# Kernel tuning notes

Measured on AMD Instinct MI355X. Metric: run time of the kernel, lower is better.

Reference implementation:

```python
import jax, jax.numpy as jnp
import numpy as np

SEQ_LEN = 8192
D_K = 128
NEG_BIG = 1000000000.0


def setup_inputs() -> dict:
    key = jax.random.key(0)
    kq, kk, kv = jax.random.split(key, 3)
    q = jax.random.normal(kq, (SEQ_LEN, D_K), dtype=jnp.float32)
    k = jax.random.normal(kk, (SEQ_LEN, D_K), dtype=jnp.float32)
    v = jax.random.normal(kv, (SEQ_LEN, D_K), dtype=jnp.float32)
    return {"q": q, "k": k, "v": v}


def reference(q, k, v):
    # q,k,v: (S, d). Naive attention with causal (look-ahead) mask, masked=True.
    d_k = q.shape[-1]
    scaled_logits = jnp.matmul(q, k.T) / jnp.sqrt(jnp.asarray(d_k, q.dtype))  # (S, S)
    look_ahead_mask = jnp.triu(jnp.ones((SEQ_LEN, SEQ_LEN), dtype=q.dtype), k=1)
    scaled_logits = scaled_logits - look_ahead_mask * NEG_BIG
    attn = jnp.matmul(jax.nn.softmax(scaled_logits, axis=-1), v)  # (S, d)
    return attn
```

## Files before the change

kernel.cpp:

```cpp
#include <hip/hip_runtime.h>
#include <hip/hip_bf16.h>
#include <math.h>

#define S_LEN 8192
#define DK    128
#define BM    64
#define BN    64
#define NQT   (S_LEN / BM)
#define SCALE 0.08838834764831845f

typedef __bf16 bf16x8_t __attribute__((ext_vector_type(8)));
typedef __bf16 bf16x4_t __attribute__((ext_vector_type(4)));
typedef float  floatx4  __attribute__((ext_vector_type(4)));

#define GLD16(g, l) __builtin_amdgcn_global_load_lds(                      \
    (const __attribute__((address_space(1))) void*)(g),                    \
    (__attribute__((address_space(3))) void*)(l), 16, 0, 0)

__global__ __launch_bounds__(256) void prep_k(const float* __restrict__ K,
                                              __bf16* __restrict__ Kb) {
  const int i = (blockIdx.x * 256 + threadIdx.x) * 4;
  float4 v = *(const float4*)&K[i];
  bf16x4_t b;
  b[0] = (__bf16)v.x; b[1] = (__bf16)v.y; b[2] = (__bf16)v.z; b[3] = (__bf16)v.w;
  *(bf16x4_t*)&Kb[i] = b;
}

__global__ __launch_bounds__(256) void prep_vt(const float* __restrict__ V,
                                               __bf16* __restrict__ Vt) {
  __shared__ __bf16 t[64][DK + 8];
  const int tid  = threadIdx.x;
  const int key0 = blockIdx.x * 64;
  {
    const int r = tid >> 2, cg = (tid & 3) * 32;
    const float* vp = V + (size_t)(key0 + r) * DK + cg;
    #pragma unroll
    for (int i = 0; i < 8; ++i) {
      float4 v = ((const float4*)vp)[i];
      bf16x4_t b;
      b[0] = (__bf16)v.x; b[1] = (__bf16)v.y; b[2] = (__bf16)v.z; b[3] = (__bf16)v.w;
      *(bf16x4_t*)&t[r][cg + i * 4] = b;
    }
  }
  __syncthreads();
  const int d = tid >> 1, h = (tid & 1) * 32;
  __bf16* op = Vt + (size_t)d * S_LEN + key0 + h;
  #pragma unroll
  for (int jb = 0; jb < 4; ++jb) {
    bf16x8_t b;
    #pragma unroll
    for (int j = 0; j < 8; ++j) b[j] = t[h + jb * 8 + j][d];
    *(bf16x8_t*)&op[jb * 8] = b;
  }
}

__global__ __launch_bounds__(256, 3)
void fa_part(const float* __restrict__ Q, const __bf16* __restrict__ Kb,
             const __bf16* __restrict__ Vtg, float* __restrict__ Opart,
             float* __restrict__ stats, int G, int direct) {
  __shared__ __align__(16) __bf16 Ks[BN * DK];
  __shared__ __align__(16) __bf16 Vts[DK * BN];
  __shared__ __align__(16) __bf16 Pl[4][16][BN + 8];

  const int tid  = threadIdx.x;
  const int wave = tid >> 6;
  const int lane = tid & 63;
  const int l15  = lane & 15;
  const int quad = lane >> 4;

  const int qtile = blockIdx.x;
  const int g     = blockIdx.y;
  const int nt    = qtile + 1;
  const int Ci    = (nt + G - 1) / G;
  const int jb0   = g * Ci;
  const int jb1   = (jb0 + Ci < nt) ? (jb0 + Ci) : nt;
  const int chunk = qtile * G + g;

  if (jb0 >= jb1) {
    if (tid < BM) {
      stats[((size_t)chunk * BM + tid) * 2 + 0] = -INFINITY;
      stats[((size_t)chunk * BM + tid) * 2 + 1] = 0.f;
    }
    return;
  }

  const int q0w = qtile * BM + wave * 16;

  bf16x8_t qf[4];
  {
    const float* qrow = Q + (size_t)(q0w + l15) * DK + quad * 8;
    #pragma unroll
    for (int kb = 0; kb < 4; ++kb) {
      const float4* p = (const float4*)(qrow + kb * 32);
      float4 a = p[0], b = p[1];
      bf16x8_t f;
      f[0]=(__bf16)a.x; f[1]=(__bf16)a.y; f[2]=(__bf16)a.z; f[3]=(__bf16)a.w;
      f[4]=(__bf16)b.x; f[5]=(__bf16)b.y; f[6]=(__bf16)b.z; f[7]=(__bf16)b.w;
      qf[kb] = f;
    }
  }

  const __bf16* kp[4]; const __bf16* vp[4];
  __bf16* kl[4]; __bf16* vl[4];
  {
    const int ck = l15 ^ ((wave * 4 + (lane >> 4)) & 15);
    const int cv = (lane & 7) ^ ((lane >> 3) & 7);
    #pragma unroll
    for (int t = 0; t < 4; ++t) {
      const int rk = t * 16 + wave * 4 + (lane >> 4);
      kp[t] = Kb + ((size_t)(jb0 * BN + rk)) * DK + ck * 8;
      kl[t] = &Ks[t * 2048 + wave * 512];
      const int rv = t * 32 + wave * 8 + (lane >> 3);
      vp[t] = Vtg + (size_t)rv * S_LEN + jb0 * BN + cv * 8;
      vl[t] = &Vts[t * 2048 + wave * 512];
    }
  }

  floatx4 o_acc[8];
  #pragma unroll
  for (int dt = 0; dt < 8; ++dt) o_acc[dt] = (floatx4){0.f, 0.f, 0.f, 0.f};
  float m_r[4], l_r[4];
  #pragma unroll
  for (int r = 0; r < 4; ++r) { m_r[r] = -INFINITY; l_r[r] = 0.f; }

  for (int jb = jb0; jb < jb1; ++jb) {
    const int key0 = jb * BN;

    #pragma unroll
    for (int t = 0; t < 4; ++t) {
      GLD16(kp[t], kl[t]);
      GLD16(vp[t], vl[t]);
      kp[t] += BN * DK;
      vp[t] += BN;
    }
    __syncthreads();

    floatx4 sv[4];
    #pragma unroll
    for (int n = 0; n < 4; ++n) {
      floatx4 acc = (floatx4){0.f, 0.f, 0.f, 0.f};
      #pragma unroll
      for (int kb = 0; kb < 4; ++kb) {
        bf16x8_t bfr = *(const bf16x8_t*)
            &Ks[(n * 16 + l15) * DK + (((kb * 4 + quad) ^ l15) * 8)];
        acc = __builtin_amdgcn_mfma_f32_16x16x32_bf16(qf[kb], bfr, acc, 0, 0, 0);
      }
      sv[n] = acc;
    }

    if (jb == qtile) {
      #pragma unroll
      for (int n = 0; n < 4; ++n) {
        const int key = key0 + n * 16 + l15;
        #pragma unroll
        for (int r = 0; r < 4; ++r) {
          const int qi = q0w + quad * 4 + r;
          float v = sv[n][r] * SCALE;
          sv[n][r] = (key > qi) ? -1e30f : v;
        }
      }
    } else {
      #pragma unroll
      for (int n = 0; n < 4; ++n)
        #pragma unroll
        for (int r = 0; r < 4; ++r) sv[n][r] *= SCALE;
    }

    float rm[4];
    #pragma unroll
    for (int r = 0; r < 4; ++r)
      rm[r] = fmaxf(fmaxf(sv[0][r], sv[1][r]), fmaxf(sv[2][r], sv[3][r]));
    #pragma unroll
    for (int off = 8; off >= 1; off >>= 1) {
      #pragma unroll
      for (int r = 0; r < 4; ++r) rm[r] = fmaxf(rm[r], __shfl_xor(rm[r], off));
    }
    float alpha[4];
    #pragma unroll
    for (int r = 0; r < 4; ++r) {
      const float mn = fmaxf(m_r[r], rm[r]);
      alpha[r] = __expf(m_r[r] - mn);
      m_r[r] = mn;
    }
    float rs[4] = {0.f, 0.f, 0.f, 0.f};
    #pragma unroll
    for (int n = 0; n < 4; ++n) {
      #pragma unroll
      for (int r = 0; r < 4; ++r) {
        const float p = __expf(sv[n][r] - m_r[r]);
        sv[n][r] = p;
        rs[r] += p;
      }
    }
    #pragma unroll
    for (int off = 8; off >= 1; off >>= 1) {
      #pragma unroll
      for (int r = 0; r < 4; ++r) rs[r] += __shfl_xor(rs[r], off);
    }
    #pragma unroll
    for (int r = 0; r < 4; ++r) l_r[r] = l_r[r] * alpha[r] + rs[r];
    #pragma unroll
    for (int dt = 0; dt < 8; ++dt)
      #pragma unroll
      for (int r = 0; r < 4; ++r) o_acc[dt][r] *= alpha[r];

    #pragma unroll
    for (int n = 0; n < 4; ++n)
      #pragma unroll
      for (int r = 0; r < 4; ++r)
        Pl[wave][quad * 4 + r][n * 16 + l15] = (__bf16)sv[n][r];
    __syncthreads();

    #pragma unroll
    for (int kc = 0; kc < 2; ++kc) {
      bf16x8_t af = *(const bf16x8_t*)&Pl[wave][l15][kc * 32 + quad * 8];
      #pragma unroll
      for (int dt = 0; dt < 8; ++dt) {
        bf16x8_t vf = *(const bf16x8_t*)
            &Vts[(dt * 16 + l15) * BN + (((kc * 4 + quad) ^ (l15 & 7)) * 8)];
        o_acc[dt] = __builtin_amdgcn_mfma_f32_16x16x32_bf16(af, vf, o_acc[dt], 0, 0, 0);
      }
    }
    __syncthreads();
  }

  if (direct) {
    #pragma unroll
    for (int r = 0; r < 4; ++r) {
      const float inv = 1.0f / l_r[r];
      float* orow = Opart + (size_t)(q0w + quad * 4 + r) * DK + l15;
      #pragma unroll
      for (int dt = 0; dt < 8; ++dt) orow[dt * 16] = o_acc[dt][r] * inv;
    }
  } else {
    #pragma unroll
    for (int r = 0; r < 4; ++r) {
      const int row = wave * 16 + quad * 4 + r;
      float* orow = Opart + ((size_t)chunk * BM + row) * DK + l15;
      #pragma unroll
      for (int dt = 0; dt < 8; ++dt) orow[dt * 16] = o_acc[dt][r];
    }
    if (l15 == 0) {
      #pragma unroll
      for (int r = 0; r < 4; ++r) {
        const int row = wave * 16 + quad * 4 + r;
        stats[((size_t)chunk * BM + row) * 2 + 0] = m_r[r];
        stats[((size_t)chunk * BM + row) * 2 + 1] = l_r[r];
      }
    }
  }
}

__global__ __launch_bounds__(256)
void fa_reduce(const float* __restrict__ Opart, const float* __restrict__ stats,
               float* __restrict__ O, int G) {
  const int wave = threadIdx.x >> 6, lane = threadIdx.x & 63;
  const int row = blockIdx.x * 4 + wave;
  const int qt = row >> 6, r = row & 63;

  float M = -INFINITY;
  for (int g = 0; g < G; ++g)
    M = fmaxf(M, stats[((size_t)(qt * G + g) * BM + r) * 2]);

  float L = 0.f;
  float ax = 0.f, ay = 0.f;
  for (int g = 0; g < G; ++g) {
    const size_t sidx = (size_t)(qt * G + g) * BM + r;
    const float m = stats[sidx * 2];
    if (m == -INFINITY) continue;
    const float w = __expf(m - M);
    L += stats[sidx * 2 + 1] * w;
    float2 o = *(const float2*)&Opart[sidx * DK + lane * 2];
    ax += w * o.x; ay += w * o.y;
  }
  const float inv = 1.f / L;
  float2 res; res.x = ax * inv; res.y = ay * inv;
  *(float2*)&O[(size_t)row * DK + lane * 2] = res;
}

extern "C" void kernel_launch(void* const* d_in, const int* in_sizes, int n_in,
                              void* d_out, int out_size, void* d_ws, size_t ws_size,
                              hipStream_t stream) {
  (void)in_sizes; (void)n_in; (void)out_size;
  const float* q = (const float*)d_in[0];
  const float* k = (const float*)d_in[1];
  const float* v = (const float*)d_in[2];
  float* out = (float*)d_out;

  const size_t conv_bytes = (size_t)S_LEN * DK * 2 * 2;
  const size_t per_g = (size_t)NQT * (BM * DK + 2 * BM) * 4;
  int G = 1;
  if (ws_size > conv_bytes + per_g) {
    G = (int)((ws_size - conv_bytes) / per_g);
    if (G > 8) G = 8;
  }

  __bf16* Kb = (__bf16*)d_ws;
  __bf16* Vt = Kb + (size_t)S_LEN * DK;
  float* Opart = (float*)(Vt + (size_t)S_LEN * DK);
  float* stats = Opart + (size_t)NQT * G * BM * DK;

  prep_k<<<(S_LEN * DK) / (256 * 4), 256, 0, stream>>>(k, Kb);
  prep_vt<<<S_LEN / 64, 256, 0, stream>>>(v, Vt);

  if (G >= 2) {
    fa_part<<<dim3(NQT, G), 256, 0, stream>>>(q, Kb, Vt, Opart, stats, G, 0);
    fa_reduce<<<S_LEN / 4, 256, 0, stream>>>(Opart, stats, out, G);
  } else {
    fa_part<<<dim3(NQT, 1), 256, 0, stream>>>(q, Kb, Vt, out, out, 1, 1);
  }
}
```

Before: 137.0 us.

## Fixed-size key chunks, K double-buffering, exp2 softmax, lazy rescale, fused prep

Splits each query tile's key range into fixed-size chunks of C tiles rather than G equal splits, launching heaviest tiles first. K is double-buffered in LDS so the next tile's load overlaps compute. Softmax switches to exp2 with the log2e factor folded into the scale, rescales only when some row max grows, and computes row sums via an MFMA against a ones vector. It also fuses the K and V prep kernels, adds s_setprio around MFMA blocks, and drops occupancy hint to 2, trading extra LDS for overlap.

```diff
diff --git a/kernel.cpp b/kernel.cpp
--- a/kernel.cpp
+++ b/kernel.cpp
@@ -7,7 +7,7 @@
 #define BM    64
 #define BN    64
 #define NQT   (S_LEN / BM)
-#define SCALE 0.08838834764831845f
+#define SCALE2 (0.08838834764831845f * 1.4426950408889634f)
 
 typedef __bf16 bf16x8_t __attribute__((ext_vector_type(8)));
 typedef __bf16 bf16x4_t __attribute__((ext_vector_type(4)));
@@ -17,20 +17,30 @@
     (const __attribute__((address_space(1))) void*)(g),                    \
     (__attribute__((address_space(3))) void*)(l), 16, 0, 0)
 
-__global__ __launch_bounds__(256) void prep_k(const float* __restrict__ K,
-                                              __bf16* __restrict__ Kb) {
-  const int i = (blockIdx.x * 256 + threadIdx.x) * 4;
-  float4 v = *(const float4*)&K[i];
-  bf16x4_t b;
-  b[0] = (__bf16)v.x; b[1] = (__bf16)v.y; b[2] = (__bf16)v.z; b[3] = (__bf16)v.w;
-  *(bf16x4_t*)&Kb[i] = b;
-}
-
-__global__ __launch_bounds__(256) void prep_vt(const float* __restrict__ V,
+__device__ __forceinline__ float fexp2(float x) {
+#if __has_builtin(__builtin_amdgcn_exp2f)
+  return __builtin_amdgcn_exp2f(x);
+#else
+  return exp2f(x);
+#endif
+}
+
+__global__ __launch_bounds__(256) void prep_kv(const float* __restrict__ K,
+                                               const float* __restrict__ V,
+                                               __bf16* __restrict__ Kb,
                                                __bf16* __restrict__ Vt) {
   __shared__ __bf16 t[64][DK + 8];
-  const int tid  = threadIdx.x;
-  const int key0 = blockIdx.x * 64;
+  const int bx  = blockIdx.x;
+  const int tid = threadIdx.x;
+  if (bx < (S_LEN * DK) / (256 * 4)) {
+    const int i = (bx * 256 + tid) * 4;
+    float4 v = *(const float4*)&K[i];
+    bf16x4_t b;
+    b[0] = (__bf16)v.x; b[1] = (__bf16)v.y; b[2] = (__bf16)v.z; b[3] = (__bf16)v.w;
+    *(bf16x4_t*)&Kb[i] = b;
+    return;
+  }
+  const int key0 = (bx - (S_LEN * DK) / (256 * 4)) * 64;
   {
     const int r = tid >> 2, cg = (tid & 3) * 32;
     const float* vp = V + (size_t)(key0 + r) * DK + cg;
@@ -54,12 +64,12 @@
   }
 }
 
-__global__ __launch_bounds__(256, 3)
+__global__ __launch_bounds__(256, 2)
 void fa_part(const float* __restrict__ Q, const __bf16* __restrict__ Kb,
              const __bf16* __restrict__ Vtg, float* __restrict__ Opart,
-             float* __restrict__ stats, int G, int direct) {
-  __shared__ __align__(16) __bf16 Ks[BN * DK];
-  __shared__ __align__(16) __bf16 Vts[DK * BN];
+             float* __restrict__ stats, int C, int direct) {
+  __shared__ __align__(16) __bf16 Ks[2][BN * DK];
+  __shared__ __align__(16) __bf16 Vts[BN * DK];
   __shared__ __align__(16) __bf16 Pl[4][16][BN + 8];
 
   const int tid  = threadIdx.x;
@@ -68,21 +78,15 @@
   const int l15  = lane & 15;
   const int quad = lane >> 4;
 
-  const int qtile = blockIdx.x;
+  const int qtile = (NQT - 1) - blockIdx.x;
   const int g     = blockIdx.y;
   const int nt    = qtile + 1;
-  const int Ci    = (nt + G - 1) / G;
-  const int jb0   = g * Ci;
-  const int jb1   = (jb0 + Ci < nt) ? (jb0 + Ci) : nt;
-  const int chunk = qtile * G + g;
-
-  if (jb0 >= jb1) {
-    if (tid < BM) {
-      stats[((size_t)chunk * BM + tid) * 2 + 0] = -INFINITY;
-      stats[((size_t)chunk * BM + tid) * 2 + 1] = 0.f;
-    }
-    return;
-  }
+  const int ca    = qtile / C;
+  if (g > ca) return;
+  const int cr  = qtile - ca * C;
+  const int jb0 = g * C;
+  const int jb1 = (jb0 + C < nt) ? (jb0 + C) : nt;
+  const int chunk = qtile + C * (ca * (ca - 1) / 2) + cr * ca + g;
 
   const int q0w = qtile * BM + wave * 16;
 
@@ -100,19 +104,17 @@
     }
   }
 
-  const __bf16* kp[4]; const __bf16* vp[4];
-  __bf16* kl[4]; __bf16* vl[4];
+  const __bf16* kp[4]; const __bf16* vp[4]; int loff[4];
   {
-    const int ck = l15 ^ ((wave * 4 + (lane >> 4)) & 15);
+    const int ck = l15 ^ ((wave * 4 + quad) & 15);
     const int cv = (lane & 7) ^ ((lane >> 3) & 7);
     #pragma unroll
     for (int t = 0; t < 4; ++t) {
-      const int rk = t * 16 + wave * 4 + (lane >> 4);
+      const int rk = t * 16 + wave * 4 + quad;
       kp[t] = Kb + ((size_t)(jb0 * BN + rk)) * DK + ck * 8;
-      kl[t] = &Ks[t * 2048 + wave * 512];
       const int rv = t * 32 + wave * 8 + (lane >> 3);
       vp[t] = Vtg + (size_t)rv * S_LEN + jb0 * BN + cv * 8;
-      vl[t] = &Vts[t * 2048 + wave * 512];
+      loff[t] = t * 2048 + wave * 512;
     }
   }
 
@@ -123,47 +125,56 @@
   #pragma unroll
   for (int r = 0; r < 4; ++r) { m_r[r] = -INFINITY; l_r[r] = 0.f; }
 
+  bf16x8_t onesf;
+  #pragma unroll
+  for (int j = 0; j < 8; ++j) onesf[j] = (__bf16)1.0f;
+
+  #pragma unroll
+  for (int t = 0; t < 4; ++t) { GLD16(kp[t], &Ks[0][loff[t]]); kp[t] += BN * DK; }
+  __syncthreads();
+
+  int bsel = 0;
   for (int jb = jb0; jb < jb1; ++jb) {
-    const int key0 = jb * BN;
-
-    #pragma unroll
-    for (int t = 0; t < 4; ++t) {
-      GLD16(kp[t], kl[t]);
-      GLD16(vp[t], vl[t]);
-      kp[t] += BN * DK;
-      vp[t] += BN;
-    }
-    __syncthreads();
+    if (jb + 1 < jb1) {
+      #pragma unroll
+      for (int t = 0; t < 4; ++t) { GLD16(kp[t], &Ks[bsel ^ 1][loff[t]]); kp[t] += BN * DK; }
+    }
+    #pragma unroll
+    for (int t = 0; t < 4; ++t) { GLD16(vp[t], &Vts[loff[t]]); vp[t] += BN; }
+
+    const __bf16* Kcur = Ks[bsel];
 
     floatx4 sv[4];
+    __builtin_amdgcn_s_setprio(1);
     #pragma unroll
     for (int n = 0; n < 4; ++n) {
       floatx4 acc = (floatx4){0.f, 0.f, 0.f, 0.f};
       #pragma unroll
       for (int kb = 0; kb < 4; ++kb) {
         bf16x8_t bfr = *(const bf16x8_t*)
-            &Ks[(n * 16 + l15) * DK + (((kb * 4 + quad) ^ l15) * 8)];
+            &Kcur[(n * 16 + l15) * DK + (((kb * 4 + quad) ^ l15) * 8)];
         acc = __builtin_amdgcn_mfma_f32_16x16x32_bf16(qf[kb], bfr, acc, 0, 0, 0);
       }
       sv[n] = acc;
     }
+    __builtin_amdgcn_s_setprio(0);
 
     if (jb == qtile) {
       #pragma unroll
       for (int n = 0; n < 4; ++n) {
-        const int key = key0 + n * 16 + l15;
+        const int key = jb * BN + n * 16 + l15;
         #pragma unroll
         for (int r = 0; r < 4; ++r) {
           const int qi = q0w + quad * 4 + r;
-          float v = sv[n][r] * SCALE;
-          sv[n][r] = (key > qi) ? -1e30f : v;
+          const float vv = sv[n][r] * SCALE2;
+          sv[n][r] = (key > qi) ? -1e30f : vv;
         }
       }
     } else {
       #pragma unroll
       for (int n = 0; n < 4; ++n)
         #pragma unroll
-        for (int r = 0; r < 4; ++r) sv[n][r] *= SCALE;
+        for (int r = 0; r < 4; ++r) sv[n][r] *= SCALE2;
     }
 
     float rm[4];
@@ -175,45 +186,38 @@
       #pragma unroll
       for (int r = 0; r < 4; ++r) rm[r] = fmaxf(rm[r], __shfl_xor(rm[r], off));
     }
-    float alpha[4];
-    #pragma unroll
-    for (int r = 0; r < 4; ++r) {
-      const float mn = fmaxf(m_r[r], rm[r]);
-      alpha[r] = __expf(m_r[r] - mn);
-      m_r[r] = mn;
-    }
-    float rs[4] = {0.f, 0.f, 0.f, 0.f};
-    #pragma unroll
-    for (int n = 0; n < 4; ++n) {
+
+    const int grow = (rm[0] > m_r[0]) || (rm[1] > m_r[1]) ||
+                     (rm[2] > m_r[2]) || (rm[3] > m_r[3]);
+    if (__any(grow)) {
+      float al[4];
       #pragma unroll
       for (int r = 0; r < 4; ++r) {
-        const float p = __expf(sv[n][r] - m_r[r]);
-        sv[n][r] = p;
-        rs[r] += p;
-      }
-    }
-    #pragma unroll
-    for (int off = 8; off >= 1; off >>= 1) {
-      #pragma unroll
-      for (int r = 0; r < 4; ++r) rs[r] += __shfl_xor(rs[r], off);
-    }
-    #pragma unroll
-    for (int r = 0; r < 4; ++r) l_r[r] = l_r[r] * alpha[r] + rs[r];
-    #pragma unroll
-    for (int dt = 0; dt < 8; ++dt)
-      #pragma unroll
-      for (int r = 0; r < 4; ++r) o_acc[dt][r] *= alpha[r];
+        const float mn = fmaxf(m_r[r], rm[r]);
+        al[r] = fexp2(m_r[r] - mn);
+        m_r[r] = mn;
+        l_r[r] *= al[r];
+      }
+      #pragma unroll
+      for (int dt = 0; dt < 8; ++dt)
+        #pragma unroll
+        for (int r = 0; r < 4; ++r) o_acc[dt][r] *= al[r];
+    }
 
     #pragma unroll
     for (int n = 0; n < 4; ++n)
       #pragma unroll
       for (int r = 0; r < 4; ++r)
-        Pl[wave][quad * 4 + r][n * 16 + l15] = (__bf16)sv[n][r];
+        Pl[wave][quad * 4 + r][n * 16 + l15] = (__bf16)fexp2(sv[n][r] - m_r[r]);
+
     __syncthreads();
 
+    floatx4 lacc = (floatx4){0.f, 0.f, 0.f, 0.f};
+    __builtin_amdgcn_s_setprio(1);
     #pragma unroll
     for (int kc = 0; kc < 2; ++kc) {
       bf16x8_t af = *(const bf16x8_t*)&Pl[wave][l15][kc * 32 + quad * 8];
+      lacc = __builtin_amdgcn_mfma_f32_16x16x32_bf16(af, onesf, lacc, 0, 0, 0);
       #pragma unroll
       for (int dt = 0; dt < 8; ++dt) {
         bf16x8_t vf = *(const bf16x8_t*)
@@ -221,7 +225,12 @@
         o_acc[dt] = __builtin_amdgcn_mfma_f32_16x16x32_bf16(af, vf, o_acc[dt], 0, 0, 0);
       }
     }
+    __builtin_amdgcn_s_setprio(0);
+    #pragma unroll
+    for (int r = 0; r < 4; ++r) l_r[r] += lacc[r];
+
     __syncthreads();
+    bsel ^= 1;
   }
 
   if (direct) {
@@ -253,22 +262,24 @@
 
 __global__ __launch_bounds__(256)
 void fa_reduce(const float* __restrict__ Opart, const float* __restrict__ stats,
-               float* __restrict__ O, int G) {
+               float* __restrict__ O, int C) {
   const int wave = threadIdx.x >> 6, lane = threadIdx.x & 63;
   const int row = blockIdx.x * 4 + wave;
   const int qt = row >> 6, r = row & 63;
 
+  const int ca = qt / C, cr = qt - ca * C;
+  const int base = qt + C * (ca * (ca - 1) / 2) + cr * ca;
+  const int nch = ca + 1;
+
   float M = -INFINITY;
-  for (int g = 0; g < G; ++g)
-    M = fmaxf(M, stats[((size_t)(qt * G + g) * BM + r) * 2]);
-
-  float L = 0.f;
-  float ax = 0.f, ay = 0.f;
-  for (int g = 0; g < G; ++g) {
-    const size_t sidx = (size_t)(qt * G + g) * BM + r;
+  for (int g = 0; g < nch; ++g)
+    M = fmaxf(M, stats[((size_t)(base + g) * BM + r) * 2]);
+
+  float L = 0.f, ax = 0.f, ay = 0.f;
+  for (int g = 0; g < nch; ++g) {
+    const size_t sidx = (size_t)(base + g) * BM + r;
     const float m = stats[sidx * 2];
-    if (m == -INFINITY) continue;
-    const float w = __expf(m - M);
+    const float w = fexp2(m - M);
     L += stats[sidx * 2 + 1] * w;
     float2 o = *(const float2*)&Opart[sidx * DK + lane * 2];
     ax += w * o.x; ay += w * o.y;
@@ -288,25 +299,28 @@
   float* out = (float*)d_out;
 
   const size_t conv_bytes = (size_t)S_LEN * DK * 2 * 2;
-  const size_t per_g = (size_t)NQT * (BM * DK + 2 * BM) * 4;
-  int G = 1;
-  if (ws_size > conv_bytes + per_g) {
-    G = (int)((ws_size - conv_bytes) / per_g);
-    if (G > 8) G = 8;
+  const size_t per_chunk  = (size_t)(BM * DK + 2 * BM) * 4;
+
+  int C = 0; long long nc = 0;
+  for (int c = 8; c <= NQT; ++c) {
+    const int a = NQT / c, rr = NQT % c;
+    const long long n = (long long)NQT + (long long)c * a * (a - 1) / 2 +
+                        (long long)rr * a;
+    if (conv_bytes + (size_t)n * per_chunk <= ws_size) { C = c; nc = n; break; }
   }
 
   __bf16* Kb = (__bf16*)d_ws;
   __bf16* Vt = Kb + (size_t)S_LEN * DK;
-  float* Opart = (float*)(Vt + (size_t)S_LEN * DK);
-  float* stats = Opart + (size_t)NQT * G * BM * DK;
-
-  prep_k<<<(S_LEN * DK) / (256 * 4), 256, 0, stream>>>(k, Kb);
-  prep_vt<<<S_LEN / 64, 256, 0, stream>>>(v, Vt);
-
-  if (G >= 2) {
-    fa_part<<<dim3(NQT, G), 256, 0, stream>>>(q, Kb, Vt, Opart, stats, G, 0);
-    fa_reduce<<<S_LEN / 4, 256, 0, stream>>>(Opart, stats, out, G);
+
+  prep_kv<<<(S_LEN * DK) / (256 * 4) + S_LEN / 64, 256, 0, stream>>>(k, v, Kb, Vt);
+
+  if (C) {
+    float* Opart = (float*)(Vt + (size_t)S_LEN * DK);
+    float* stats = Opart + (size_t)nc * BM * DK;
+    const int gy = (NQT - 1) / C + 1;
+    fa_part<<<dim3(NQT, gy), 256, 0, stream>>>(q, Kb, Vt, Opart, stats, C, 0);
+    fa_reduce<<<S_LEN / 4, 256, 0, stream>>>(Opart, stats, out, C);
   } else {
-    fa_part<<<dim3(NQT, 1), 256, 0, stream>>>(q, Kb, Vt, out, out, 1, 1);
-  }
-}
+    fa_part<<<dim3(NQT, 1), 256, 0, stream>>>(q, Kb, Vt, out, out, NQT, 1);
+  }
+}
```

Result: no change. 136.6 us (-0.3%).
